# Optimization experiments

Hardware: AMD Instinct MI355X
Metric: run time of the kernel (lower is better)

Reference implementation:

```python
import jax, jax.numpy as jnp
import numpy as np
from jax import lax

T_ITERS = 6
LN_EPS = 1e-5

def layer_norm(x, g, b):
    mu = jnp.mean(x, axis=-1, keepdims=True)
    var = jnp.var(x, axis=-1, keepdims=True)
    return (x - mu) * lax.rsqrt(var + LN_EPS) * g + b

def setup_inputs() -> dict:
    key = jax.random.key(0)
    ks = jax.random.split(key, 12)
    B, C_in, S = 8, 128, 33
    hidden = 2 * C_in          # 256
    dim = 256                  # feat_dim
    N = 64
    w = lambda k, shp, s=0.02: (jax.random.normal(k, shp, jnp.float32) * s)
    return {
        "x": jax.random.normal(ks[0], (B, C_in, S, S, S), jnp.float32),
        "templates_init": jax.random.normal(ks[1], (1, N, dim), jnp.float32),
        "conv_w": w(ks[2], (hidden, C_in, 3, 3, 3)),
        "conv_b": jnp.zeros((hidden,), jnp.float32),
        "Wq": w(ks[3], (dim, dim)),
        "Wk": w(ks[4], (hidden, dim)),
        "Wv": w(ks[5], (hidden, dim)),
        "ln_in_g": jnp.ones((hidden,), jnp.float32), "ln_in_b": jnp.zeros((hidden,), jnp.float32),
        "ln_t_g": jnp.ones((dim,), jnp.float32),    "ln_t_b": jnp.zeros((dim,), jnp.float32),
        "ln_m_g": jnp.ones((dim,), jnp.float32),    "ln_m_b": jnp.zeros((dim,), jnp.float32),
        "W1": w(ks[6], (dim, 2 * dim)), "b1": jnp.zeros((2 * dim,), jnp.float32),
        "W2": w(ks[7], (2 * dim, dim)), "b2": jnp.zeros((dim,), jnp.float32),
    }

def reference(x, templates_init, conv_w, conv_b, Wq, Wk, Wv,
              ln_in_g, ln_in_b, ln_t_g, ln_t_b, ln_m_g, ln_m_b,
              W1, b1, W2, b2):
    # project: Conv3d stride 2, no padding, + ReLU
    h = lax.conv_general_dilated(x, conv_w, window_strides=(2, 2, 2),
                                 padding='VALID',
                                 dimension_numbers=('NCDHW', 'OIDHW', 'NCDHW'))
    h = jax.nn.relu(h + conv_b[None, :, None, None, None])
    B, C, X, Y, Z = h.shape
    dim = templates_init.shape[-1]
    N = templates_init.shape[1]
    scale = dim ** (-0.5)
    tokens = h.reshape(B, C, X * Y * Z).transpose(0, 2, 1)   # (B, L, hidden)
    tokens = layer_norm(tokens, ln_in_g, ln_in_b)
    k = tokens @ Wk                                           # (B, L, dim)
    v = tokens @ Wv                                           # (B, L, dim)
    templates = jnp.broadcast_to(templates_init, (B, N, dim))
    attn = None
    for _ in range(T_ITERS):
        t_prev = templates
        t = layer_norm(templates, ln_t_g, ln_t_b)
        q = (t @ Wq) * scale                                  # (B, N, dim)
        attn_logits = jnp.einsum('bnd,bld->bln', q, k)        # (B, L, N)
        attn = jax.nn.softmax(attn_logits, axis=-1)           # competitive over N
        attn = attn + 1e-8
        attn = attn / jnp.sum(attn, axis=-2, keepdims=True)   # renormalize over L
        templates = t_prev + jnp.einsum('bld,bln->bnd', v, attn)
        m = layer_norm(templates, ln_m_g, ln_m_b)
        templates = templates + (jax.nn.gelu(m @ W1 + b1, approximate=False) @ W2 + b2)
    templates_out = templates.transpose(0, 2, 1)              # (B, dim, N)
    attn_out = attn.transpose(0, 2, 1).reshape(B, N, X, Y, Z)
    return templates_out, attn_out
```

## Files before the change

### kernel.cpp

```cpp
#include <hip/hip_runtime.h>

typedef unsigned short u16;
typedef short s16x8 __attribute__((ext_vector_type(8)));
typedef float f32x4 __attribute__((ext_vector_type(4)));
typedef float f32x4u __attribute__((ext_vector_type(4), aligned(4)));
typedef unsigned short us4 __attribute__((ext_vector_type(4)));

__device__ __forceinline__ float bf2f(u16 v) {
    return __uint_as_float(((unsigned int)v) << 16);
}
__device__ __forceinline__ u16 f2bf(float f) {
    unsigned int u = __float_as_uint(f);
    u = u + 0x7FFFu + ((u >> 16) & 1u);
    return (u16)(u >> 16);
}
__device__ __forceinline__ f32x4 mfma16(s16x8 a, s16x8 b, f32x4 c) {
    return __builtin_amdgcn_mfma_f32_16x16x32_bf16(a, b, c, 0, 0, 0);
}
#define ZERO4 f32x4{0.f, 0.f, 0.f, 0.f}

__global__ void prepack_kernel(const float* __restrict__ conv_w, const float* __restrict__ Wk,
                               const float* __restrict__ Wv, const float* __restrict__ Wq,
                               const float* __restrict__ W1, const float* __restrict__ W2,
                               u16* __restrict__ Bp, u16* __restrict__ WkvP, u16* __restrict__ WqP,
                               u16* __restrict__ W1T, u16* __restrict__ W2T)
{
    int idx = blockIdx.x * 256 + threadIdx.x;
    if (idx < 294912) {
        int n = idx / 1152, g = idx - n * 1152;
        int ic = g / 9, r = g - ic * 9;
        const float* s = conv_w + n * 3456 + ic * 27 + r * 3;
        u16* d = Bp + n * 4608 + g * 4;
        d[0] = f2bf(s[0]); d[1] = f2bf(s[1]); d[2] = f2bf(s[2]); d[3] = 0;
    } else if (idx < 425984) {
        int i = idx - 294912;
        int n = i >> 8, c = i & 255;
        WkvP[i] = f2bf((n < 256) ? Wk[c * 256 + n] : Wv[c * 256 + (n - 256)]);
    } else if (idx < 491520) {
        int i = idx - 425984;
        int n = i >> 8, c = i & 255;
        WqP[i] = f2bf(Wq[c * 256 + n]);
    } else if (idx < 622592) {
        int i = idx - 491520;
        int h = i >> 8, c = i & 255;
        W1T[i] = f2bf(W1[c * 512 + h]);
    } else if (idx < 753664) {
        int i = idx - 622592;
        int dd = i >> 9, h = i & 511;
        W2T[i] = f2bf(W2[h * 256 + dd]);
    }
}

__global__ __launch_bounds__(512, 4) void conv_fused(
    const float* __restrict__ x, const u16* __restrict__ Bp, const float* __restrict__ conv_b,
    const float* __restrict__ ln_g, const float* __restrict__ ln_b, const u16* __restrict__ WkvP,
    u16* __restrict__ kbuf, u16* __restrict__ vT)
{
    __shared__ __align__(16) char smem[66816];
    u16* slab0  = (u16*)smem;
    u16* slab1  = (u16*)(smem + 31104);
    u16* tokbf  = (u16*)smem;
    float* lnred  = (float*)(smem + 62208);
    float* lnstat = (float*)(smem + 66304);

    int blk = blockIdx.x;
    int b = blk & 7, ox = (blk >> 5) & 15, oyb = (blk >> 3) & 3;
    int tid = threadIdx.x, wid = tid >> 6, lane = tid & 63;
    int quad = lane >> 4, l15 = lane & 15;
    int nbase = wid * 32;

    f32x4 acc[4][2];
    #pragma unroll
    for (int i = 0; i < 4; ++i)
        #pragma unroll
        for (int j = 0; j < 2; ++j) acc[i][j] = ZERO4;

    const u16* bprow0 = Bp + (nbase + l15) * 4608 + quad * 8;
    const u16* bprow1 = bprow0 + 16 * 4608;

    const float* xp[8]; int so8[8]; unsigned wmask = 0;
    #pragma unroll
    for (int u = 0; u < 8; ++u) {
        int s = tid + u * 512;
        so8[u] = -1; xp[u] = x;
        if (s < 3888) {
            int row = s / 9;
            int c = s - row * 9;
            int icl = row / 27;
            int rr = row - icl * 27;
            int ixl = rr / 9;
            int iyl = rr - ixl * 9;
            const float* xr = x + ((size_t)((b * 128 + icl) * 33) + (2 * ox + ixl)) * 1089
                              + (8 * oyb + iyl) * 33;
            if (c < 8) { xp[u] = xr + c * 4; wmask |= (1u << u); }
            else       { xp[u] = xr + 32; }
            so8[u] = row * 36 + c * 4;
        }
    }
    const size_t ICST = 16ull * 35937;

    f32x4u tv[8];
#define LOADX(ICC)                                                          \
    {                                                                       \
        _Pragma("unroll")                                                   \
        for (int u = 0; u < 8; ++u) {                                       \
            if (so8[u] >= 0) {                                              \
                const float* p = xp[u] + (size_t)(ICC) * ICST;              \
                if ((wmask >> u) & 1u) tv[u] = *(const f32x4u*)p;           \
                else                   tv[u] = f32x4u{p[0], 0.f, 0.f, 0.f}; \
            }                                                               \
        }                                                                   \
    }
#define STOREX(DST)                                                         \
    {                                                                       \
        _Pragma("unroll")                                                   \
        for (int u = 0; u < 8; ++u) {                                       \
            if (so8[u] >= 0) {                                              \
                us4 w;                                                      \
                w.x = f2bf(tv[u].x); w.y = f2bf(tv[u].y);                   \
                w.z = f2bf(tv[u].z); w.w = f2bf(tv[u].w);                   \
                *(us4*)((DST) + so8[u]) = w;                                \
            }                                                               \
        }                                                                   \
    }

    LOADX(0)
    STOREX(slab0)
    __syncthreads();

    for (int icc = 0; icc < 8; ++icc) {
        const u16* cur = (icc & 1) ? slab1 : slab0;
        u16* nxt = (icc & 1) ? slab0 : slab1;
        if (icc < 7) LOADX(icc + 1)

        const u16* bk0 = bprow0 + icc * 576;
        const u16* bk1 = bprow1 + icc * 576;
        s16x8 bbA[2], bbB[2];
        bbA[0] = *reinterpret_cast<const s16x8*>(bk0);
        bbA[1] = *reinterpret_cast<const s16x8*>(bk1);

#define CONV_STEP(CC, BREG)                                                     \
        {                                                                       \
            int g = (CC) * 8 + quad * 2;                                        \
            int i0 = g / 9, r9 = g - i0 * 9;                                    \
            int kx = r9 / 3, ky = r9 - kx * 3;                                  \
            int base0 = (i0 * 27 + kx * 9 + ky) * 36 + 2 * l15;                 \
            g += 1;                                                             \
            i0 = g / 9; r9 = g - i0 * 9; kx = r9 / 3; ky = r9 - kx * 3;         \
            int base1 = (i0 * 27 + kx * 9 + ky) * 36 + 2 * l15;                 \
            _Pragma("unroll")                                                   \
            for (int fm = 0; fm < 4; ++fm) {                                    \
                union { s16x8 v; ushort2 h[4]; } af;                            \
                const u16* sp0 = cur + base0 + fm * 72;                         \
                const u16* sp1 = cur + base1 + fm * 72;                         \
                af.h[0] = *(const ushort2*)(sp0);                               \
                af.h[1] = *(const ushort2*)(sp0 + 2);                           \
                af.h[2] = *(const ushort2*)(sp1);                               \
                af.h[3] = *(const ushort2*)(sp1 + 2);                           \
                acc[fm][0] = mfma16(af.v, (BREG)[0], acc[fm][0]);               \
                acc[fm][1] = mfma16(af.v, (BREG)[1], acc[fm][1]);               \
            }                                                                   \
        }

        #pragma unroll 1
        for (int c8 = 0; c8 < 18; c8 += 2) {
            bbB[0] = *reinterpret_cast<const s16x8*>(bk0 + (c8 + 1) * 32);
            bbB[1] = *reinterpret_cast<const s16x8*>(bk1 + (c8 + 1) * 32);
            CONV_STEP(c8, bbA)
            if (c8 + 2 < 18) {
                bbA[0] = *reinterpret_cast<const s16x8*>(bk0 + (c8 + 2) * 32);
                bbA[1] = *reinterpret_cast<const s16x8*>(bk1 + (c8 + 2) * 32);
            }
            CONV_STEP(c8 + 1, bbB)
        }
#undef CONV_STEP
        if (icc < 7) STOREX(nxt)
        __syncthreads();
    }
#undef LOADX
#undef STOREX

    #pragma unroll
    for (int fn = 0; fn < 2; ++fn) {
        float bias = conv_b[nbase + fn * 16 + l15];
        #pragma unroll
        for (int fm = 0; fm < 4; ++fm)
            #pragma unroll
            for (int r = 0; r < 4; ++r)
                acc[fm][fn][r] = fmaxf(acc[fm][fn][r] + bias, 0.f);
    }
    #pragma unroll
    for (int fm = 0; fm < 4; ++fm) {
        #pragma unroll
        for (int r = 0; r < 4; ++r) {
            float s = acc[fm][0][r] + acc[fm][1][r];
            float q2 = acc[fm][0][r] * acc[fm][0][r] + acc[fm][1][r] * acc[fm][1][r];
            #pragma unroll
            for (int msk = 1; msk <= 8; msk <<= 1) {
                s  += __shfl_xor(s, msk, 64);
                q2 += __shfl_xor(q2, msk, 64);
            }
            if (l15 == 0) {
                int mm = fm * 16 + quad * 4 + r;
                lnred[(wid * 64 + mm) * 2 + 0] = s;
                lnred[(wid * 64 + mm) * 2 + 1] = q2;
            }
        }
    }
    __syncthreads();
    if (tid < 64) {
        float s = 0, q2 = 0;
        #pragma unroll
        for (int w = 0; w < 8; ++w) { s += lnred[(w * 64 + tid) * 2]; q2 += lnred[(w * 64 + tid) * 2 + 1]; }
        float mu = s * (1.f / 256.f);
        float var = fmaxf(q2 * (1.f / 256.f) - mu * mu, 0.f);
        lnstat[tid * 2]     = mu;
        lnstat[tid * 2 + 1] = rsqrtf(var + 1e-5f);
    }
    __syncthreads();
    {
        float gam[2], bet[2];
        #pragma unroll
        for (int fn = 0; fn < 2; ++fn) {
            int n = nbase + fn * 16 + l15;
            gam[fn] = ln_g[n]; bet[fn] = ln_b[n];
        }
        #pragma unroll
        for (int fm = 0; fm < 4; ++fm)
            #pragma unroll
            for (int r = 0; r < 4; ++r) {
                int mm = fm * 16 + quad * 4 + r;
                float mu = lnstat[mm * 2], rs = lnstat[mm * 2 + 1];
                #pragma unroll
                for (int fn = 0; fn < 2; ++fn) {
                    int n = nbase + fn * 16 + l15;
                    tokbf[mm * 264 + n] = f2bf((acc[fm][fn][r] - mu) * rs * gam[fn] + bet[fn]);
                }
            }
    }
    __syncthreads();
    f32x4 kacc[4][4];
    #pragma unroll
    for (int i = 0; i < 4; ++i)
        #pragma unroll
        for (int j = 0; j < 4; ++j) kacc[i][j] = ZERO4;
    int n2 = wid * 64;
    const u16* wp = WkvP + (n2 + l15) * 256 + quad * 8;
    s16x8 wvA[4], wvB[4];
    #pragma unroll
    for (int fn = 0; fn < 4; ++fn) wvA[fn] = *reinterpret_cast<const s16x8*>(wp + fn * 4096);

#define KV_STEP(KK, WREG)                                                           \
    {                                                                               \
        s16x8 a2[4];                                                                \
        _Pragma("unroll")                                                           \
        for (int fm = 0; fm < 4; ++fm)                                              \
            a2[fm] = *reinterpret_cast<const s16x8*>(tokbf + (fm * 16 + l15) * 264  \
                                                     + (KK) * 32 + quad * 8);       \
        _Pragma("unroll")                                                           \
        for (int fn = 0; fn < 4; ++fn)                                              \
            _Pragma("unroll")                                                       \
            for (int fm = 0; fm < 4; ++fm)                                          \
                kacc[fm][fn] = mfma16(a2[fm], (WREG)[fn], kacc[fm][fn]);            \
    }

    #pragma unroll 1
    for (int kc = 0; kc < 8; kc += 2) {
        #pragma unroll
        for (int fn = 0; fn < 4; ++fn)
            wvB[fn] = *reinterpret_cast<const s16x8*>(wp + fn * 4096 + (kc + 1) * 32);
        KV_STEP(kc, wvA)
        if (kc + 2 < 8) {
            #pragma unroll
            for (int fn = 0; fn < 4; ++fn)
                wvA[fn] = *reinterpret_cast<const s16x8*>(wp + fn * 4096 + (kc + 2) * 32);
        }
        KV_STEP(kc + 1, wvB)
    }
#undef KV_STEP

    #pragma unroll
    for (int fm = 0; fm < 4; ++fm)
        #pragma unroll
        for (int r = 0; r < 4; ++r) {
            int l = (ox * 16 + oyb * 4 + fm) * 16 + quad * 4 + r;
            #pragma unroll
            for (int fn = 0; fn < 4; ++fn) {
                int n = n2 + fn * 16 + l15;
                u16 v = f2bf(kacc[fm][fn][r]);
                if (n < 256) kbuf[((b << 12) + l) * 256 + n] = v;
                else         vT[((b * 256 + (n - 256)) << 12) + l] = v;
            }
        }
}

__global__ __launch_bounds__(256) void kQ(
    const float* __restrict__ tinit, float* __restrict__ tpl,
    const float* __restrict__ ln_t_g, const float* __restrict__ ln_t_b,
    const u16* __restrict__ WqP, u16* __restrict__ qbuf, float* __restrict__ delta)
{
    __shared__ __align__(16) u16 mls[64 * 264];
    __shared__ float pls[64][4][2];
    __shared__ float stat[64][2];
    int b = blockIdx.x, tid = threadIdx.x;
    int m = tid >> 2, part = tid & 3;
    const float* tp = tinit + m * 256 + part * 64;
    float* tg = tpl + (b * 64 + m) * 256 + part * 64;
    float s = 0, q2 = 0;
    for (int i = 0; i < 64; ++i) {
        float v = tp[i];
        tg[i] = v;
        s += v; q2 += v * v;
    }
    pls[m][part][0] = s; pls[m][part][1] = q2;
    __syncthreads();
    if (tid < 64) {
        float ss = 0, qq = 0;
        #pragma unroll
        for (int p = 0; p < 4; ++p) { ss += pls[tid][p][0]; qq += pls[tid][p][1]; }
        float mu = ss * (1.f / 256.f);
        float var = fmaxf(qq * (1.f / 256.f) - mu * mu, 0.f);
        stat[tid][0] = mu; stat[tid][1] = rsqrtf(var + 1e-5f);
    }
    __syncthreads();
    {
        float mu = stat[m][0], rs = stat[m][1];
        for (int i = 0; i < 64; ++i) {
            int d = part * 64 + i;
            mls[m * 264 + d] = f2bf((tp[i] - mu) * rs * ln_t_g[d] + ln_t_b[d]);
        }
    }
    __syncthreads();
    int wid = tid >> 6, lane = tid & 63, quad = lane >> 4, l15 = lane & 15;
    f32x4 qa[4][4];
    #pragma unroll
    for (int i = 0; i < 4; ++i)
        #pragma unroll
        for (int j = 0; j < 4; ++j) qa[i][j] = ZERO4;
    #pragma unroll 1
    for (int kc = 0; kc < 8; ++kc) {
        s16x8 a[4];
        #pragma unroll
        for (int fm = 0; fm < 4; ++fm)
            a[fm] = *reinterpret_cast<const s16x8*>(mls + (fm * 16 + l15) * 264 + kc * 32 + quad * 8);
        #pragma unroll
        for (int fn = 0; fn < 4; ++fn) {
            s16x8 bv = *reinterpret_cast<const s16x8*>(WqP + (wid * 64 + fn * 16 + l15) * 256 + kc * 32 + quad * 8);
            #pragma unroll
            for (int fm = 0; fm < 4; ++fm)
                qa[fm][fn] = mfma16(a[fm], bv, qa[fm][fn]);
        }
    }
    #pragma unroll
    for (int fm = 0; fm < 4; ++fm)
        #pragma unroll
        for (int fn = 0; fn < 4; ++fn)
            #pragma unroll
            for (int r = 0; r < 4; ++r) {
                int mt = fm * 16 + quad * 4 + r;
                int d = wid * 64 + fn * 16 + l15;
                qbuf[(b * 64 + mt) * 256 + d] = f2bf(qa[fm][fn][r] * 0.0625f);
            }
    f32x4* dz = (f32x4*)(delta + b * 16384);
    for (int i = tid; i < 4096; i += 256) dz[i] = ZERO4;
}

__global__ __launch_bounds__(512, 2) void kA(
    const u16* __restrict__ qbuf, const u16* __restrict__ kbuf, const u16* __restrict__ vT,
    float* __restrict__ cs_part, float* __restrict__ delta, int last, u16* __restrict__ attnT)
{
    __shared__ __align__(16) u16 qls[64 * 264];
    __shared__ __align__(16) u16 atile[64 * 136];
    __shared__ float colsh[8][64];
    int b = blockIdx.x & 7, ltg = blockIdx.x >> 3;
    int tid = threadIdx.x, wid = tid >> 6, lane = tid & 63;
    int quad = lane >> 4, l15 = lane & 15;

    {
        int r = tid >> 3, c = (tid & 7) * 32;
        const u16* src = qbuf + b * 16384 + r * 256 + c;
        u16* dst = qls + r * 264 + c;
        #pragma unroll
        for (int j = 0; j < 4; ++j)
            *(int4*)(dst + j * 8) = *(const int4*)(src + j * 8);
    }
    int lrow = ltg * 128 + wid * 16;
    const u16* arow = kbuf + (size_t)((b << 12) + lrow + l15) * 256;
    s16x8 av[8];
    #pragma unroll
    for (int kc = 0; kc < 8; ++kc)
        av[kc] = *reinterpret_cast<const s16x8*>(arow + kc * 32 + quad * 8);
    const u16* vrow = vT + ((size_t)(b * 256 + wid * 32 + l15) << 12) + ltg * 128 + quad * 8;
    s16x8 bv2[2][4];
    #pragma unroll
    for (int fn = 0; fn < 2; ++fn)
        #pragma unroll
        for (int kc = 0; kc < 4; ++kc)
            bv2[fn][kc] = *reinterpret_cast<const s16x8*>(vrow + (fn << 16) + kc * 32);
    __syncthreads();
    f32x4 sa[4];
    #pragma unroll
    for (int fn = 0; fn < 4; ++fn) sa[fn] = ZERO4;
    #pragma unroll
    for (int kc = 0; kc < 8; ++kc) {
        #pragma unroll
        for (int fn = 0; fn < 4; ++fn) {
            s16x8 bv = *reinterpret_cast<const s16x8*>(qls + (fn * 16 + l15) * 264 + kc * 32 + quad * 8);
            sa[fn] = mfma16(av[kc], bv, sa[fn]);
        }
    }
    float colp[4] = {0.f, 0.f, 0.f, 0.f};
    #pragma unroll
    for (int r = 0; r < 4; ++r) {
        float mx = fmaxf(fmaxf(sa[0][r], sa[1][r]), fmaxf(sa[2][r], sa[3][r]));
        #pragma unroll
        for (int msk = 1; msk <= 8; msk <<= 1) mx = fmaxf(mx, __shfl_xor(mx, msk, 64));
        float e[4], sum = 0;
        #pragma unroll
        for (int fn = 0; fn < 4; ++fn) { e[fn] = __expf(sa[fn][r] - mx); sum += e[fn]; }
        #pragma unroll
        for (int msk = 1; msk <= 8; msk <<= 1) sum += __shfl_xor(sum, msk, 64);
        float inv = 1.f / sum;
        #pragma unroll
        for (int fn = 0; fn < 4; ++fn) {
            float p = e[fn] * inv + 1e-8f;
            colp[fn] += p;
            atile[(fn * 16 + l15) * 136 + wid * 16 + quad * 4 + r] = f2bf(p);
        }
    }
    #pragma unroll
    for (int fn = 0; fn < 4; ++fn) {
        float c = colp[fn];
        c += __shfl_xor(c, 16, 64);
        c += __shfl_xor(c, 32, 64);
        if (lane < 16) colsh[wid][fn * 16 + lane] = c;
    }
    __syncthreads();
    if (tid < 64) {
        float s = 0;
        #pragma unroll
        for (int w = 0; w < 8; ++w) s += colsh[w][tid];
        cs_part[((b << 5) + ltg) * 64 + tid] = s;
    }
    {
        f32x4 pacc[4][2];
        #pragma unroll
        for (int i = 0; i < 4; ++i)
            #pragma unroll
            for (int j = 0; j < 2; ++j) pacc[i][j] = ZERO4;
        #pragma unroll
        for (int kc = 0; kc < 4; ++kc) {
            #pragma unroll
            for (int fm = 0; fm < 4; ++fm) {
                s16x8 a = *reinterpret_cast<const s16x8*>(atile + (fm * 16 + l15) * 136 + kc * 32 + quad * 8);
                #pragma unroll
                for (int fn = 0; fn < 2; ++fn)
                    pacc[fm][fn] = mfma16(a, bv2[fn][kc], pacc[fm][fn]);
            }
        }
        #pragma unroll
        for (int fm = 0; fm < 4; ++fm)
            #pragma unroll
            for (int fn = 0; fn < 2; ++fn)
                #pragma unroll
                for (int r = 0; r < 4; ++r) {
                    int n = fm * 16 + quad * 4 + r;
                    int d = wid * 32 + fn * 16 + l15;
                    atomicAdd(&delta[(size_t)(b * 64 + n) * 256 + d], pacc[fm][fn][r]);
                }
    }
    if (last) {
        int n = tid >> 3, lo = (tid & 7) * 16;
        const u16* src = atile + n * 136 + lo;
        u16* dst = attnT + (size_t)((b * 64 + n) << 12) + ltg * 128 + lo;
        *(int4*)(dst)     = *(const int4*)(src);
        *(int4*)(dst + 8) = *(const int4*)(src + 8);
    }
}

__global__ __launch_bounds__(512) void kT(
    float* __restrict__ tpl, float* __restrict__ delta, const float* __restrict__ cs_part,
    float* __restrict__ colsum,
    const float* __restrict__ ln_m_g, const float* __restrict__ ln_m_b,
    const u16* __restrict__ W1T, const float* __restrict__ b1,
    const u16* __restrict__ W2T, const float* __restrict__ b2,
    const float* __restrict__ ln_t_g, const float* __restrict__ ln_t_b,
    const u16* __restrict__ WqP, u16* __restrict__ qbuf,
    int last, float* __restrict__ out0)
{
    __shared__ __align__(16) u16 mls[16 * 264];
    __shared__ __align__(16) u16 hid[16 * 520];
    __shared__ float pls[16][32][2];
    __shared__ float stat[16][2];
    __shared__ float lnr2[8][16][2];
    __shared__ float csh[16];
    int b = blockIdx.x & 7, mg = blockIdx.x >> 3;
    int m0 = mg * 16;
    int tid = threadIdx.x, wid = tid >> 6, lane = tid & 63;
    int quad = lane >> 4, l15 = lane & 15;
    if (tid < 16) {
        float s = 0;
        #pragma unroll
        for (int g = 0; g < 32; ++g) s += cs_part[((b << 5) + g) * 64 + m0 + tid];
        csh[tid] = 1.f / s;
        if (last) colsum[b * 64 + m0 + tid] = s;
    }
    __syncthreads();
    {
        int ml = tid >> 5, part = tid & 31;
        float cinv = csh[ml];
        float* tg = tpl + (b * 64 + m0 + ml) * 256 + part * 8;
        float* dg = delta + (size_t)(b * 64 + m0 + ml) * 256 + part * 8;
        float vbuf[8];
        float s = 0, q2 = 0;
        #pragma unroll
        for (int i = 0; i < 8; ++i) {
            float v = tg[i] + dg[i] * cinv;
            vbuf[i] = v; s += v; q2 += v * v;
        }
        if (!last) {
            f32x4* dz = (f32x4*)dg;
            dz[0] = ZERO4; dz[1] = ZERO4;
        }
        pls[ml][part][0] = s; pls[ml][part][1] = q2;
        __syncthreads();
        if (tid < 16) {
            float ss = 0, qq = 0;
            #pragma unroll
            for (int p = 0; p < 32; ++p) { ss += pls[tid][p][0]; qq += pls[tid][p][1]; }
            float mu = ss * (1.f / 256.f);
            float var = fmaxf(qq * (1.f / 256.f) - mu * mu, 0.f);
            stat[tid][0] = mu; stat[tid][1] = rsqrtf(var + 1e-5f);
        }
        __syncthreads();
        float mu = stat[ml][0], rs = stat[ml][1];
        #pragma unroll
        for (int i = 0; i < 8; ++i) {
            int d = part * 8 + i;
            tg[i] = vbuf[i];
            mls[ml * 264 + d] = f2bf((vbuf[i] - mu) * rs * ln_m_g[d] + ln_m_b[d]);
        }
    }
    __syncthreads();
    {
        f32x4 ha[4];
        #pragma unroll
        for (int j = 0; j < 4; ++j) ha[j] = ZERO4;
        #pragma unroll 1
        for (int kc = 0; kc < 8; ++kc) {
            s16x8 a = *reinterpret_cast<const s16x8*>(mls + l15 * 264 + kc * 32 + quad * 8);
            #pragma unroll
            for (int fn = 0; fn < 4; ++fn) {
                s16x8 bv = *reinterpret_cast<const s16x8*>(W1T + (wid * 64 + fn * 16 + l15) * 256 + kc * 32 + quad * 8);
                ha[fn] = mfma16(a, bv, ha[fn]);
            }
        }
        #pragma unroll
        for (int fn = 0; fn < 4; ++fn) {
            int nh = wid * 64 + fn * 16 + l15;
            float bb = b1[nh];
            #pragma unroll
            for (int r = 0; r < 4; ++r) {
                float v = ha[fn][r] + bb;
                v = 0.5f * v * (1.f + erff(v * 0.70710678118654752f));
                hid[(quad * 4 + r) * 520 + nh] = f2bf(v);
            }
        }
    }
    __syncthreads();
    {
        f32x4 oa[2];
        oa[0] = ZERO4; oa[1] = ZERO4;
        #pragma unroll 1
        for (int kc = 0; kc < 16; ++kc) {
            s16x8 a = *reinterpret_cast<const s16x8*>(hid + l15 * 520 + kc * 32 + quad * 8);
            #pragma unroll
            for (int fn = 0; fn < 2; ++fn) {
                s16x8 bv = *reinterpret_cast<const s16x8*>(W2T + (wid * 32 + fn * 16 + l15) * 512 + kc * 32 + quad * 8);
                oa[fn] = mfma16(a, bv, oa[fn]);
            }
        }
        #pragma unroll
        for (int fn = 0; fn < 2; ++fn) {
            int d = wid * 32 + fn * 16 + l15;
            float bb = b2[d];
            #pragma unroll
            for (int r = 0; r < 4; ++r) {
                int mm = quad * 4 + r;
                oa[fn][r] += bb + tpl[(b * 64 + m0 + mm) * 256 + d];
            }
        }
        #pragma unroll
        for (int r = 0; r < 4; ++r) {
            float s = oa[0][r] + oa[1][r];
            float q2 = oa[0][r] * oa[0][r] + oa[1][r] * oa[1][r];
            #pragma unroll
            for (int msk = 1; msk <= 8; msk <<= 1) {
                s  += __shfl_xor(s, msk, 64);
                q2 += __shfl_xor(q2, msk, 64);
            }
            if (l15 == 0) {
                lnr2[wid][quad * 4 + r][0] = s;
                lnr2[wid][quad * 4 + r][1] = q2;
            }
        }
        __syncthreads();
        if (tid < 16) {
            float ss = 0, qq = 0;
            #pragma unroll
            for (int w = 0; w < 8; ++w) { ss += lnr2[w][tid][0]; qq += lnr2[w][tid][1]; }
            float mu = ss * (1.f / 256.f);
            float var = fmaxf(qq * (1.f / 256.f) - mu * mu, 0.f);
            stat[tid][0] = mu; stat[tid][1] = rsqrtf(var + 1e-5f);
        }
        __syncthreads();
        #pragma unroll
        for (int fn = 0; fn < 2; ++fn) {
            int d = wid * 32 + fn * 16 + l15;
            float gg = last ? 0.f : ln_t_g[d];
            float bt = last ? 0.f : ln_t_b[d];
            #pragma unroll
            for (int r = 0; r < 4; ++r) {
                int mm = quad * 4 + r;
                float v = oa[fn][r];
                tpl[(b * 64 + m0 + mm) * 256 + d] = v;
                if (last) {
                    out0[(b * 256 + d) * 64 + m0 + mm] = v;
                } else {
                    mls[mm * 264 + d] = f2bf((v - stat[mm][0]) * stat[mm][1] * gg + bt);
                }
            }
        }
    }
    if (!last) {
        __syncthreads();
        f32x4 qa[2];
        qa[0] = ZERO4; qa[1] = ZERO4;
        #pragma unroll 1
        for (int kc = 0; kc < 8; ++kc) {
            s16x8 a = *reinterpret_cast<const s16x8*>(mls + l15 * 264 + kc * 32 + quad * 8);
            #pragma unroll
            for (int fn = 0; fn < 2; ++fn) {
                s16x8 bv = *reinterpret_cast<const s16x8*>(WqP + (wid * 32 + fn * 16 + l15) * 256 + kc * 32 + quad * 8);
                qa[fn] = mfma16(a, bv, qa[fn]);
            }
        }
        #pragma unroll
        for (int fn = 0; fn < 2; ++fn)
            #pragma unroll
            for (int r = 0; r < 4; ++r) {
                int mt = m0 + quad * 4 + r;
                int d = wid * 32 + fn * 16 + l15;
                qbuf[(b * 64 + mt) * 256 + d] = f2bf(qa[fn][r] * 0.0625f);
            }
    }
}

__global__ void kE(const u16* __restrict__ attnT, const float* __restrict__ colsum,
                   float* __restrict__ out1)
{
    int blk = blockIdx.x;
    int b = blk & 7, r8 = blk >> 3;
    int e = (b << 18) + (r8 << 10) + threadIdx.x * 4;
    int n = (e >> 12) & 63;
    float ci = 1.f / colsum[b * 64 + n];
    const u16* s = attnT + e;
    f32x4 o;
    o.x = bf2f(s[0]) * ci; o.y = bf2f(s[1]) * ci;
    o.z = bf2f(s[2]) * ci; o.w = bf2f(s[3]) * ci;
    *(f32x4*)(out1 + e) = o;
}

extern "C" void kernel_launch(void* const* d_in, const int* in_sizes, int n_in,
                              void* d_out, int out_size, void* d_ws, size_t ws_size,
                              hipStream_t stream)
{
    const float* x       = (const float*)d_in[0];
    const float* tinit   = (const float*)d_in[1];
    const float* conv_w  = (const float*)d_in[2];
    const float* conv_b  = (const float*)d_in[3];
    const float* Wq      = (const float*)d_in[4];
    const float* Wk      = (const float*)d_in[5];
    const float* Wv      = (const float*)d_in[6];
    const float* ln_in_g = (const float*)d_in[7];
    const float* ln_in_b = (const float*)d_in[8];
    const float* ln_t_g  = (const float*)d_in[9];
    const float* ln_t_b  = (const float*)d_in[10];
    const float* ln_m_g  = (const float*)d_in[11];
    const float* ln_m_b  = (const float*)d_in[12];
    const float* W1      = (const float*)d_in[13];
    const float* b1      = (const float*)d_in[14];
    const float* W2      = (const float*)d_in[15];
    const float* b2      = (const float*)d_in[16];

    char* ws = (char*)d_ws;
    u16* Bp       = (u16*)(ws + 0);
    u16* WkvP     = (u16*)(ws + 2359296);
    u16* WqP      = (u16*)(ws + 2621440);
    u16* W1T      = (u16*)(ws + 2752512);
    u16* W2T      = (u16*)(ws + 3014656);
    u16* kbuf     = (u16*)(ws + 3276800);
    u16* vT       = (u16*)(ws + 20054016);
    u16* qbuf     = (u16*)(ws + 36831232);
    u16* attnT    = (u16*)(ws + 37093376);
    float* colsum = (float*)(ws + 41287680);
    float* tpl    = (float*)(ws + 41289728);
    float* delta  = (float*)(ws + 41814016);
    float* cs_part= (float*)(ws + 42338304);

    float* out0 = (float*)d_out;
    float* out1 = out0 + 131072;

    prepack_kernel<<<2944, 256, 0, stream>>>(conv_w, Wk, Wv, Wq, W1, W2, Bp, WkvP, WqP, W1T, W2T);
    conv_fused<<<512, 512, 0, stream>>>(x, Bp, conv_b, ln_in_g, ln_in_b, WkvP, kbuf, vT);
    kQ<<<8, 256, 0, stream>>>(tinit, tpl, ln_t_g, ln_t_b, WqP, qbuf, delta);
    for (int it = 0; it < 6; ++it) {
        int last = (it == 5) ? 1 : 0;
        kA<<<256, 512, 0, stream>>>(qbuf, kbuf, vT, cs_part, delta, last, attnT);
        kT<<<32, 512, 0, stream>>>(tpl, delta, cs_part, colsum, ln_m_g, ln_m_b, W1T, b1, W2T, b2,
                                   ln_t_g, ln_t_b, WqP, qbuf, last, out0);
    }
    kE<<<2048, 256, 0, stream>>>(attnT, colsum, out1);
}
```

Measured before the change: 716.8 us.

## Double kA wavefronts per block and fold attention output scaling into kT

```diff
diff --git a/kernel.cpp b/kernel.cpp
--- a/kernel.cpp
+++ b/kernel.cpp
@@ -365,128 +365,142 @@
     for (int i = tid; i < 4096; i += 256) dz[i] = ZERO4;
 }
 
-__global__ __launch_bounds__(512, 2) void kA(
+__global__ __launch_bounds__(1024, 1) void kA(
     const u16* __restrict__ qbuf, const u16* __restrict__ kbuf, const u16* __restrict__ vT,
     float* __restrict__ cs_part, float* __restrict__ delta, int last, u16* __restrict__ attnT)
 {
     __shared__ __align__(16) u16 qls[64 * 264];
     __shared__ __align__(16) u16 atile[64 * 136];
-    __shared__ float colsh[8][64];
+    __shared__ float colsh[64][8];
+    __shared__ float smx[8][2][16];
+    __shared__ float ssm[8][2][16];
     int b = blockIdx.x & 7, ltg = blockIdx.x >> 3;
     int tid = threadIdx.x, wid = tid >> 6, lane = tid & 63;
     int quad = lane >> 4, l15 = lane & 15;
+    int rowgrp = wid & 7, fnh = wid >> 3;
 
     {
-        int r = tid >> 3, c = (tid & 7) * 32;
+        int r = tid >> 4, c = (tid & 15) * 16;
         const u16* src = qbuf + b * 16384 + r * 256 + c;
         u16* dst = qls + r * 264 + c;
-        #pragma unroll
-        for (int j = 0; j < 4; ++j)
-            *(int4*)(dst + j * 8) = *(const int4*)(src + j * 8);
-    }
-    int lrow = ltg * 128 + wid * 16;
+        *(int4*)(dst)     = *(const int4*)(src);
+        *(int4*)(dst + 8) = *(const int4*)(src + 8);
+    }
+    int lrow = ltg * 128 + rowgrp * 16;
     const u16* arow = kbuf + (size_t)((b << 12) + lrow + l15) * 256;
     s16x8 av[8];
     #pragma unroll
     for (int kc = 0; kc < 8; ++kc)
         av[kc] = *reinterpret_cast<const s16x8*>(arow + kc * 32 + quad * 8);
-    const u16* vrow = vT + ((size_t)(b * 256 + wid * 32 + l15) << 12) + ltg * 128 + quad * 8;
-    s16x8 bv2[2][4];
-    #pragma unroll
-    for (int fn = 0; fn < 2; ++fn)
-        #pragma unroll
-        for (int kc = 0; kc < 4; ++kc)
-            bv2[fn][kc] = *reinterpret_cast<const s16x8*>(vrow + (fn << 16) + kc * 32);
-    __syncthreads();
-    f32x4 sa[4];
-    #pragma unroll
-    for (int fn = 0; fn < 4; ++fn) sa[fn] = ZERO4;
+    const u16* vrow = vT + ((size_t)(b * 256 + wid * 16 + l15) << 12) + ltg * 128 + quad * 8;
+    s16x8 bv2[4];
+    #pragma unroll
+    for (int kc = 0; kc < 4; ++kc)
+        bv2[kc] = *reinterpret_cast<const s16x8*>(vrow + kc * 32);
+    __syncthreads();
+    f32x4 sa[2];
+    sa[0] = ZERO4; sa[1] = ZERO4;
     #pragma unroll
     for (int kc = 0; kc < 8; ++kc) {
         #pragma unroll
-        for (int fn = 0; fn < 4; ++fn) {
-            s16x8 bv = *reinterpret_cast<const s16x8*>(qls + (fn * 16 + l15) * 264 + kc * 32 + quad * 8);
+        for (int fn = 0; fn < 2; ++fn) {
+            s16x8 bv = *reinterpret_cast<const s16x8*>(
+                qls + (fnh * 32 + fn * 16 + l15) * 264 + kc * 32 + quad * 8);
             sa[fn] = mfma16(av[kc], bv, sa[fn]);
         }
     }
-    float colp[4] = {0.f, 0.f, 0.f, 0.f};
+    float mx[4];
     #pragma unroll
     for (int r = 0; r < 4; ++r) {
-        float mx = fmaxf(fmaxf(sa[0][r], sa[1][r]), fmaxf(sa[2][r], sa[3][r]));
-        #pragma unroll
-        for (int msk = 1; msk <= 8; msk <<= 1) mx = fmaxf(mx, __shfl_xor(mx, msk, 64));
-        float e[4], sum = 0;
-        #pragma unroll
-        for (int fn = 0; fn < 4; ++fn) { e[fn] = __expf(sa[fn][r] - mx); sum += e[fn]; }
-        #pragma unroll
-        for (int msk = 1; msk <= 8; msk <<= 1) sum += __shfl_xor(sum, msk, 64);
-        float inv = 1.f / sum;
-        #pragma unroll
-        for (int fn = 0; fn < 4; ++fn) {
-            float p = e[fn] * inv + 1e-8f;
+        float m = fmaxf(sa[0][r], sa[1][r]);
+        #pragma unroll
+        for (int msk = 1; msk <= 8; msk <<= 1) m = fmaxf(m, __shfl_xor(m, msk, 64));
+        mx[r] = m;
+    }
+    if (l15 == 0) {
+        #pragma unroll
+        for (int r = 0; r < 4; ++r) smx[rowgrp][fnh][quad * 4 + r] = mx[r];
+    }
+    __syncthreads();
+    float e[2][4], ps[4];
+    #pragma unroll
+    for (int r = 0; r < 4; ++r) {
+        float g = fmaxf(mx[r], smx[rowgrp][1 - fnh][quad * 4 + r]);
+        e[0][r] = __expf(sa[0][r] - g);
+        e[1][r] = __expf(sa[1][r] - g);
+        float s = e[0][r] + e[1][r];
+        #pragma unroll
+        for (int msk = 1; msk <= 8; msk <<= 1) s += __shfl_xor(s, msk, 64);
+        ps[r] = s;
+    }
+    if (l15 == 0) {
+        #pragma unroll
+        for (int r = 0; r < 4; ++r) ssm[rowgrp][fnh][quad * 4 + r] = ps[r];
+    }
+    __syncthreads();
+    float colp[2] = {0.f, 0.f};
+    #pragma unroll
+    for (int r = 0; r < 4; ++r) {
+        float inv = 1.f / (ps[r] + ssm[rowgrp][1 - fnh][quad * 4 + r]);
+        #pragma unroll
+        for (int fn = 0; fn < 2; ++fn) {
+            float p = e[fn][r] * inv + 1e-8f;
             colp[fn] += p;
-            atile[(fn * 16 + l15) * 136 + wid * 16 + quad * 4 + r] = f2bf(p);
-        }
-    }
-    #pragma unroll
-    for (int fn = 0; fn < 4; ++fn) {
+            atile[(fnh * 32 + fn * 16 + l15) * 136 + rowgrp * 16 + quad * 4 + r] = f2bf(p);
+        }
+    }
+    #pragma unroll
+    for (int fn = 0; fn < 2; ++fn) {
         float c = colp[fn];
         c += __shfl_xor(c, 16, 64);
         c += __shfl_xor(c, 32, 64);
-        if (lane < 16) colsh[wid][fn * 16 + lane] = c;
+        if (lane < 16) colsh[fnh * 32 + fn * 16 + lane][rowgrp] = c;
     }
     __syncthreads();
     if (tid < 64) {
         float s = 0;
         #pragma unroll
-        for (int w = 0; w < 8; ++w) s += colsh[w][tid];
+        for (int rg = 0; rg < 8; ++rg) s += colsh[tid][rg];
         cs_part[((b << 5) + ltg) * 64 + tid] = s;
     }
     {
-        f32x4 pacc[4][2];
-        #pragma unroll
-        for (int i = 0; i < 4; ++i)
-            #pragma unroll
-            for (int j = 0; j < 2; ++j) pacc[i][j] = ZERO4;
+        f32x4 pacc[4];
+        #pragma unroll
+        for (int i = 0; i < 4; ++i) pacc[i] = ZERO4;
         #pragma unroll
         for (int kc = 0; kc < 4; ++kc) {
             #pragma unroll
             for (int fm = 0; fm < 4; ++fm) {
-                s16x8 a = *reinterpret_cast<const s16x8*>(atile + (fm * 16 + l15) * 136 + kc * 32 + quad * 8);
-                #pragma unroll
-                for (int fn = 0; fn < 2; ++fn)
-                    pacc[fm][fn] = mfma16(a, bv2[fn][kc], pacc[fm][fn]);
-            }
-        }
+                s16x8 a = *reinterpret_cast<const s16x8*>(
+                    atile + (fm * 16 + l15) * 136 + kc * 32 + quad * 8);
+                pacc[fm] = mfma16(a, bv2[kc], pacc[fm]);
+            }
+        }
+        int d = wid * 16 + l15;
         #pragma unroll
         for (int fm = 0; fm < 4; ++fm)
             #pragma unroll
-            for (int fn = 0; fn < 2; ++fn)
-                #pragma unroll
-                for (int r = 0; r < 4; ++r) {
-                    int n = fm * 16 + quad * 4 + r;
-                    int d = wid * 32 + fn * 16 + l15;
-                    atomicAdd(&delta[(size_t)(b * 64 + n) * 256 + d], pacc[fm][fn][r]);
-                }
+            for (int r = 0; r < 4; ++r) {
+                int n = fm * 16 + quad * 4 + r;
+                atomicAdd(&delta[(size_t)(b * 64 + n) * 256 + d], pacc[fm][r]);
+            }
     }
     if (last) {
-        int n = tid >> 3, lo = (tid & 7) * 16;
+        int n = tid >> 4, lo = (tid & 15) * 8;
         const u16* src = atile + n * 136 + lo;
         u16* dst = attnT + (size_t)((b * 64 + n) << 12) + ltg * 128 + lo;
-        *(int4*)(dst)     = *(const int4*)(src);
-        *(int4*)(dst + 8) = *(const int4*)(src + 8);
+        *(int4*)(dst) = *(const int4*)(src);
     }
 }
 
 __global__ __launch_bounds__(512) void kT(
     float* __restrict__ tpl, float* __restrict__ delta, const float* __restrict__ cs_part,
-    float* __restrict__ colsum,
     const float* __restrict__ ln_m_g, const float* __restrict__ ln_m_b,
     const u16* __restrict__ W1T, const float* __restrict__ b1,
     const u16* __restrict__ W2T, const float* __restrict__ b2,
     const float* __restrict__ ln_t_g, const float* __restrict__ ln_t_b,
     const u16* __restrict__ WqP, u16* __restrict__ qbuf,
-    int last, float* __restrict__ out0)
+    int last, const u16* __restrict__ attnT, float* __restrict__ out0, float* __restrict__ out1)
 {
     __shared__ __align__(16) u16 mls[16 * 264];
     __shared__ __align__(16) u16 hid[16 * 520];
@@ -503,7 +517,6 @@
         #pragma unroll
         for (int g = 0; g < 32; ++g) s += cs_part[((b << 5) + g) * 64 + m0 + tid];
         csh[tid] = 1.f / s;
-        if (last) colsum[b * 64 + m0 + tid] = s;
     }
     __syncthreads();
     {
@@ -653,22 +666,21 @@
                 int d = wid * 32 + fn * 16 + l15;
                 qbuf[(b * 64 + mt) * 256 + d] = f2bf(qa[fn][r] * 0.0625f);
             }
-    }
-}
-
-__global__ void kE(const u16* __restrict__ attnT, const float* __restrict__ colsum,
-                   float* __restrict__ out1)
-{
-    int blk = blockIdx.x;
-    int b = blk & 7, r8 = blk >> 3;
-    int e = (b << 18) + (r8 << 10) + threadIdx.x * 4;
-    int n = (e >> 12) & 63;
-    float ci = 1.f / colsum[b * 64 + n];
-    const u16* s = attnT + e;
-    f32x4 o;
-    o.x = bf2f(s[0]) * ci; o.y = bf2f(s[1]) * ci;
-    o.z = bf2f(s[2]) * ci; o.w = bf2f(s[3]) * ci;
-    *(f32x4*)(out1 + e) = o;
+    } else {
+        int n = m0 + (tid >> 5);
+        int c0 = (tid & 31) * 128;
+        float ci = csh[tid >> 5];
+        const u16* src = attnT + ((size_t)(b * 64 + n) << 12) + c0;
+        float* dst = out1 + ((size_t)(b * 64 + n) << 12) + c0;
+        #pragma unroll 4
+        for (int j = 0; j < 128; j += 4) {
+            us4 w = *(const us4*)(src + j);
+            f32x4 o;
+            o.x = bf2f(w.x) * ci; o.y = bf2f(w.y) * ci;
+            o.z = bf2f(w.z) * ci; o.w = bf2f(w.w) * ci;
+            *(f32x4*)(dst + j) = o;
+        }
+    }
 }
 
 extern "C" void kernel_launch(void* const* d_in, const int* in_sizes, int n_in,
@@ -703,7 +715,6 @@
     u16* vT       = (u16*)(ws + 20054016);
     u16* qbuf     = (u16*)(ws + 36831232);
     u16* attnT    = (u16*)(ws + 37093376);
-    float* colsum = (float*)(ws + 41287680);
     float* tpl    = (float*)(ws + 41289728);
     float* delta  = (float*)(ws + 41814016);
     float* cs_part= (float*)(ws + 42338304);
@@ -716,9 +727,8 @@
     kQ<<<8, 256, 0, stream>>>(tinit, tpl, ln_t_g, ln_t_b, WqP, qbuf, delta);
     for (int it = 0; it < 6; ++it) {
         int last = (it == 5) ? 1 : 0;
-        kA<<<256, 512, 0, stream>>>(qbuf, kbuf, vT, cs_part, delta, last, attnT);
-        kT<<<32, 512, 0, stream>>>(tpl, delta, cs_part, colsum, ln_m_g, ln_m_b, W1T, b1, W2T, b2,
-                                   ln_t_g, ln_t_b, WqP, qbuf, last, out0);
-    }
-    kE<<<2048, 256, 0, stream>>>(attnT, colsum, out1);
-}
+        kA<<<256, 1024, 0, stream>>>(qbuf, kbuf, vT, cs_part, delta, last, attnT);
+        kT<<<32, 512, 0, stream>>>(tpl, delta, cs_part, ln_m_g, ln_m_b, W1T, b1,
+                                   W2T, b2, ln_t_g, ln_t_b, WqP, qbuf, last, attnT, out0, out1);
+    }
+}
```

New measurement: 741.4 us. +3.4%, slower.
